# Optimization experiments

Measured on AMD Instinct MI355X. Metric: run time of the kernel, lower is better.

Reference implementation:

```python
import jax, jax.numpy as jnp
import numpy as np

UNITS = 256
IN_DIM = 256
OUT_DIM = 10
TOL = 1e-4
MAX_ITER = 50


def setup_inputs() -> dict:
    key = jax.random.key(0)
    ks = jax.random.split(key, 16)
    B = 65536
    s = 1.0 / np.sqrt(UNITS)
    inp = {
        "x": jax.random.normal(ks[0], (B, IN_DIM), dtype=jnp.float32),
        "w_in": jax.random.normal(ks[1], (IN_DIM, UNITS), dtype=jnp.float32) * s,
        "b_in": jax.random.normal(ks[2], (UNITS,), dtype=jnp.float32) * 0.01,
        "w_out": jax.random.normal(ks[3], (UNITS, OUT_DIM), dtype=jnp.float32) * s,
        "b_out": jax.random.normal(ks[4], (OUT_DIM,), dtype=jnp.float32) * 0.01,
    }
    eye = jnp.eye(UNITS, dtype=jnp.float32)
    for i in range(4):
        # well-conditioned (invertible) implicit-layer weight: I + small perturbation
        inp[f"w{i+1}"] = eye + 0.1 * jax.random.normal(ks[5 + 2 * i], (UNITS, UNITS), dtype=jnp.float32) * s
        inp[f"b{i+1}"] = jax.random.normal(ks[6 + 2 * i], (UNITS,), dtype=jnp.float32) * 0.01
    return inp


def newton_block(x, W, b):
    # Solve z @ W = x + tanh(x) + b by Newton iteration with early exit on ||g||.
    c = x + jnp.tanh(x) + b  # [B, n]
    z0 = x
    g0 = z0 @ W - c

    def cond(state):
        z, g, it = state
        return (it < MAX_ITER) & (jnp.linalg.norm(g) >= TOL)

    def body(state):
        z, g, it = state
        # torch.solve(g[:, :, None], W^T.repeat(B,1,1)): shared matrix -> one solve
        z = z - jnp.linalg.solve(W.T, g.T).T
        g = z @ W - c
        return (z, g, it + 1)

    z, _, _ = jax.lax.while_loop(cond, body, (z0, g0, jnp.asarray(0)))
    z = jax.lax.stop_gradient(z)  # torch loop runs under no_grad
    # final differentiable correction (torch: z = z - (z@W - x - tanh(x) - b))
    return z - (z @ W - c)


def reference(x, w_in, b_in, w1, b1, w2, b2, w3, b3, w4, b4, w_out, b_out):
    z = x @ w_in + b_in
    z = newton_block(z, w1, b1)
    z = newton_block(z, w2, b2)
    z = newton_block(z, w3, b3)
    z = newton_block(z, w4, b4)
    logits = z @ w_out + b_out
    return jax.nn.softmax(logits, axis=1)
```

## Files before the change

kernel.cpp:

```cpp
#include <hip/hip_runtime.h>
#include <hip/hip_fp16.h>
#include <math.h>


typedef __attribute__((ext_vector_type(8))) short short8;
typedef __attribute__((ext_vector_type(4))) float f32x4;

__device__ __forceinline__ float tanh_fast(float x) {
#if __has_builtin(__builtin_amdgcn_exp2f)
  float e = __builtin_amdgcn_exp2f(x * 2.8853900817779268f);
#else
  float e = __expf(2.0f * x);
#endif
  return 1.0f - 2.0f * __builtin_amdgcn_rcpf(e + 1.0f);
}
__device__ __forceinline__ unsigned rn_pair16(float v0, float v1) {
  __half2 h = __floats2half2_rn(v0, v1);
  return *reinterpret_cast<unsigned*>(&h);
}
__device__ __forceinline__ unsigned rtz_pair16(float v0, float v1) {
#if __has_builtin(__builtin_amdgcn_cvt_pkrtz)
  typedef __fp16 h2v __attribute__((ext_vector_type(2)));
  h2v h = __builtin_amdgcn_cvt_pkrtz(v0, v1);
  return *reinterpret_cast<unsigned*>(&h);
#else
  return rn_pair16(v0, v1);
#endif
}

__global__ __launch_bounds__(256) void ns_poly_k(
    const float* __restrict__ w1, const float* __restrict__ w2,
    const float* __restrict__ w3, const float* __restrict__ w4,
    const float* __restrict__ w_in, const float* __restrict__ w_out,
    unsigned* __restrict__ pk) {
  const int bid = blockIdx.x;
  const int t = threadIdx.x;
  if (bid >= 256) {
    int idx = (bid - 256) * 256 + t;
    {
      int kc = idx >> 12;
      int nt = (idx >> 8) & 15;
      int lane = (idx >> 2) & 63;
      int d = idx & 3;
      int n = nt * 16 + (lane & 15);
      int kb = kc * 32 + (lane >> 4) * 8 + d * 2;
      pk[idx] = rn_pair16(w_in[kb * 256 + n], w_in[(kb + 1) * 256 + n]);
    }
    int idx2 = idx + 32768;
    if (idx2 < 34816) {
      int r2 = idx2 - 32768;
      int kc = r2 >> 8;
      int lane = (r2 >> 2) & 63;
      int d = r2 & 3;
      int n = lane & 15;
      int kb = kc * 32 + (lane >> 4) * 8 + d * 2;
      float v0 = (n < 10) ? w_out[kb * 10 + n] : 0.0f;
      float v1 = (n < 10) ? w_out[(kb + 1) * 10 + n] : 0.0f;
      pk[5 * 32768 + r2] = rn_pair16(v0, v1);
    }
    return;
  }
  const int m = bid >> 6;
  const int r0 = (bid & 63) * 4;
  const float* __restrict__ W = (m == 0) ? w1 : (m == 1) ? w2 : (m == 2) ? w3 : w4;
  __shared__ float S[4][256];

#pragma unroll
  for (int i = 0; i < 4; ++i) {
    int e = i * 256 + t;
    int r = e >> 8, c = e & 255;
    S[r][c] = (((r0 + r) == c) ? 6.0f : 0.0f) - W[(r0 + r) * 256 + c];
  }
  __syncthreads();

  const float coef[4] = {-15.0f, 20.0f, -15.0f, 6.0f};
#pragma unroll
  for (int step = 0; step < 4; ++step) {
    float acc[4];
#pragma unroll
    for (int r = 0; r < 4; ++r) acc[r] = 0.0f;
    for (int k = 0; k < 256; k += 4) {
      float4 sv[4];
#pragma unroll
      for (int r = 0; r < 4; ++r) sv[r] = *(const float4*)&S[r][k];
      float wv0 = W[(k + 0) * 256 + t];
      float wv1 = W[(k + 1) * 256 + t];
      float wv2 = W[(k + 2) * 256 + t];
      float wv3 = W[(k + 3) * 256 + t];
#pragma unroll
      for (int r = 0; r < 4; ++r) {
        acc[r] = fmaf(sv[r].x, wv0, acc[r]);
        acc[r] = fmaf(sv[r].y, wv1, acc[r]);
        acc[r] = fmaf(sv[r].z, wv2, acc[r]);
        acc[r] = fmaf(sv[r].w, wv3, acc[r]);
      }
    }
    __syncthreads();
    float cdiag = coef[step];
#pragma unroll
    for (int r = 0; r < 4; ++r)
      S[r][t] = acc[r] + (((r0 + r) == t) ? cdiag : 0.0f);
    __syncthreads();
  }

  const int kc = r0 >> 5;
  const int quad = (r0 >> 3) & 3;
  const int d0 = (r0 & 7) >> 1;
#pragma unroll
  for (int i = 0; i < 2; ++i) {
    int q = i * 256 + t;
    int nt = q >> 5;
    int n16 = (q >> 1) & 15;
    int dd = q & 1;
    int n = nt * 16 + n16;
    int lane = quad * 16 + n16;
    unsigned word = rn_pair16(S[2 * dd][n], S[2 * dd + 1][n]);
    pk[(m + 1) * 32768 + kc * 4096 + nt * 256 + lane * 4 + (d0 + dd)] = word;
  }
}

#define MFMA_PHASE(ACC, S)                                                     \
  {                                                                            \
    const unsigned short* pl = zpl + (S) * 16384;                              \
    _Pragma("unroll") for (int mt = 0; mt < 4; ++mt)                           \
        ACC[mt] = (f32x4){0.f, 0.f, 0.f, 0.f};                                 \
    _Pragma("unroll") for (int kc = 0; kc < 8; ++kc) {                         \
      short8 zf[4];                                                            \
      _Pragma("unroll") for (int mt = 0; mt < 4; ++mt)                         \
          zf[mt] = *(const short8*)&pl[rd_base[mt] + ((rd_pm[mt] ^ (kc * 4)) * 8)]; \
      _Pragma("unroll") for (int mt = 0; mt < 4; ++mt)                         \
          ACC[mt] = __builtin_amdgcn_mfma_f32_16x16x32_f16(wreg[kc], zf[mt],   \
                                                           ACC[mt], 0, 0, 0); \
    }                                                                          \
  }

#define EPI_PHASE(ACC, S, BN, BI, DOTANH)                                      \
  {                                                                            \
    unsigned short* pl = zpl + (S) * 16384;                                    \
    float4 bn4 = make_float4(0.f, 0.f, 0.f, 0.f);                              \
    float4 bi4 = make_float4(0.f, 0.f, 0.f, 0.f);                              \
    if (DOTANH) bn4 = *(const float4*)((BN) + colb);                           \
    if ((BI) != nullptr) bi4 = *(const float4*)((BI) + colb);                  \
    _Pragma("unroll") for (int mt = 0; mt < 4; ++mt) {                         \
      float v0 = ACC[mt][0] + bi4.x;                                           \
      float v1 = ACC[mt][1] + bi4.y;                                           \
      float v2 = ACC[mt][2] + bi4.z;                                           \
      float v3 = ACC[mt][3] + bi4.w;                                           \
      if (DOTANH) {                                                            \
        v0 = v0 + tanh_fast(v0) + bn4.x;                                       \
        v1 = v1 + tanh_fast(v1) + bn4.y;                                       \
        v2 = v2 + tanh_fast(v2) + bn4.z;                                       \
        v3 = v3 + tanh_fast(v3) + bn4.w;                                       \
      }                                                                        \
      uint2 zp;                                                                \
      zp.x = rtz_pair16(v0, v1);                                               \
      zp.y = rtz_pair16(v2, v3);                                               \
      *(uint2*)&pl[wr_off[mt]] = zp;                                           \
    }                                                                          \
  }

__global__ __launch_bounds__(1024, 4) void fused2_k(
    const float* __restrict__ x, const unsigned* __restrict__ pk,
    const float* __restrict__ b_in,
    const float* __restrict__ b1, const float* __restrict__ b2,
    const float* __restrict__ b3, const float* __restrict__ b4,
    const float* __restrict__ b_out, float* __restrict__ out) {
  __shared__ unsigned short zpl[4 * 64 * 256];
  const int t = threadIdx.x;
  const int ln = t & 63;
  const int wv = t >> 6;
  const int quad = ln >> 4;
  const int n16 = ln & 15;
  const int grow0 = blockIdx.x * 256;

#pragma unroll
  for (int i = 0; i < 16; ++i) {
    int e = i * 4096 + t * 4;
    int r = e >> 8, c = e & 255;
    float4 v = *(const float4*)(x + (grow0 + r) * 256 + c);
    int g = r >> 6, rl = r & 63;
    int idx = g * 16384 + rl * 256 + (((c >> 3) ^ (rl & 31)) * 8) + (c & 7);
    uint2 zp;
    zp.x = rtz_pair16(v.x, v.y);
    zp.y = rtz_pair16(v.z, v.w);
    *(uint2*)&zpl[idx] = zp;
  }

  const int colb = wv * 16 + quad * 4;
  int rd_base[4], rd_pm[4], wr_off[4];
#pragma unroll
  for (int mt = 0; mt < 4; ++mt) {
    int mm = mt * 16 + n16;
    rd_base[mt] = mm * 256;
    rd_pm[mt] = quad ^ (mm & 31);
    wr_off[mt] = mm * 256 + (((colb >> 3) ^ (mm & 31)) * 8) + (colb & 7);
  }

  __syncthreads();

  f32x4 accA[4], accB[4];

  for (int layer = 0; layer < 5; ++layer) {
    const unsigned* pkl = pk + layer * 32768 + wv * 256 + ln * 4;
    short8 wreg[8];
#pragma unroll
    for (int kc = 0; kc < 8; ++kc) wreg[kc] = *(const short8*)(pkl + kc * 4096);

    if (layer > 0) {
      const float* bnp = (layer == 1) ? b1 : (layer == 2) ? b2 : (layer == 3) ? b3 : b4;
      const float* bip = (layer == 1) ? b_in : nullptr;
      EPI_PHASE(accB, 3, bnp, bip, true);
    }
    MFMA_PHASE(accA, 0);
    __syncthreads();

    const float* bn = (layer == 0) ? b1 : (layer == 1) ? b2 : (layer == 2) ? b3 : b4;
    const float* bi0 = (layer == 0) ? b_in : nullptr;
    const bool dt = (layer < 4);

    EPI_PHASE(accA, 0, bn, bi0, dt);
    MFMA_PHASE(accB, 1);
    __syncthreads();
    EPI_PHASE(accB, 1, bn, bi0, dt);
    MFMA_PHASE(accA, 2);
    __syncthreads();
    EPI_PHASE(accA, 2, bn, bi0, dt);
    MFMA_PHASE(accB, 3);
    __syncthreads();
  }
  EPI_PHASE(accB, 3, (const float*)nullptr, (const float*)nullptr, false);
  __syncthreads();

  {
    const int g = wv >> 2;
    const int kw = wv & 3;
    f32x4 lacc[4];
#pragma unroll
    for (int mt = 0; mt < 4; ++mt) lacc[mt] = (f32x4){0.f, 0.f, 0.f, 0.f};
    const unsigned* pw = pk + 5 * 32768 + ln * 4;
    const unsigned short* pl = zpl + g * 16384;
#pragma unroll
    for (int kk = 0; kk < 2; ++kk) {
      int kc = kw * 2 + kk;
      short8 wh = *(const short8*)(pw + kc * 256);
#pragma unroll
      for (int mt = 0; mt < 4; ++mt) {
        short8 zf = *(const short8*)&pl[rd_base[mt] + ((rd_pm[mt] ^ (kc * 4)) * 8)];
        lacc[mt] = __builtin_amdgcn_mfma_f32_16x16x32_f16(wh, zf, lacc[mt], 0, 0, 0);
      }
    }
    __syncthreads();
    float* pbuf = (float*)zpl;
#pragma unroll
    for (int mt = 0; mt < 4; ++mt) {
      int addr = g * 4096 + kw * 1024 + (mt * 16 + n16) * 16 + quad * 4;
      *(f32x4*)&pbuf[addr] = lacc[mt];
    }
    __syncthreads();
    if (t < 256) {
      int g2 = t >> 6;
      int rl = t & 63;
      float lg[10];
      float mx = -1e30f;
#pragma unroll
      for (int j = 0; j < 10; ++j) {
        float s = b_out[j];
#pragma unroll
        for (int k2 = 0; k2 < 4; ++k2) s += pbuf[g2 * 4096 + k2 * 1024 + rl * 16 + j];
        lg[j] = s;
        mx = fmaxf(mx, s);
      }
      float sum = 0.f;
#pragma unroll
      for (int j = 0; j < 10; ++j) {
        lg[j] = __expf(lg[j] - mx);
        sum += lg[j];
      }
      float inv = 1.0f / sum;
      float* op = out + (grow0 + t) * 10;
#pragma unroll
      for (int j = 0; j < 10; ++j) op[j] = lg[j] * inv;
    }
  }
}

extern "C" void kernel_launch(void* const* d_in, const int* in_sizes, int n_in,
                              void* d_out, int out_size, void* d_ws, size_t ws_size,
                              hipStream_t stream) {
  const float* x     = (const float*)d_in[0];
  const float* w_in  = (const float*)d_in[1];
  const float* b_in  = (const float*)d_in[2];
  const float* w_out = (const float*)d_in[3];
  const float* b_out = (const float*)d_in[4];
  const float* w1 = (const float*)d_in[5];
  const float* b1 = (const float*)d_in[6];
  const float* w2 = (const float*)d_in[7];
  const float* b2 = (const float*)d_in[8];
  const float* w3 = (const float*)d_in[9];
  const float* b3 = (const float*)d_in[10];
  const float* w4 = (const float*)d_in[11];
  const float* b4 = (const float*)d_in[12];
  float* out = (float*)d_out;

  unsigned* pk = (unsigned*)d_ws;

  ns_poly_k<<<384, 256, 0, stream>>>(w1, w2, w3, w4, w_in, w_out, pk);
  fused2_k<<<256, 1024, 0, stream>>>(x, pk, b_in, b1, b2, b3, b4, b_out, out);
}
```

Before: 212.9 us.

## Restructure fused kernel to 4-wave blocks with 64-column per-wave weight tiles

```diff
diff --git a/kernel.cpp b/kernel.cpp
--- a/kernel.cpp
+++ b/kernel.cpp
@@ -119,154 +119,160 @@
   }
 }
 
-#define MFMA_PHASE(ACC, S)                                                     \
+#define M_PHASE(PL)                                                            \
   {                                                                            \
-    const unsigned short* pl = zpl + (S) * 16384;                              \
     _Pragma("unroll") for (int mt = 0; mt < 4; ++mt)                           \
-        ACC[mt] = (f32x4){0.f, 0.f, 0.f, 0.f};                                 \
+      _Pragma("unroll") for (int nt = 0; nt < 4; ++nt)                         \
+        acc[mt][nt] = (f32x4){0.f, 0.f, 0.f, 0.f};                             \
     _Pragma("unroll") for (int kc = 0; kc < 8; ++kc) {                         \
       short8 zf[4];                                                            \
+      _Pragma("unroll") for (int mt = 0; mt < 4; ++mt) {                       \
+        int mm = mt * 16 + n16;                                                \
+        zf[mt] = *(const short8*)&(PL)[mm * 256 + (((kc * 4 + quad) ^ (mm & 31)) * 8)]; \
+      }                                                                        \
       _Pragma("unroll") for (int mt = 0; mt < 4; ++mt)                         \
-          zf[mt] = *(const short8*)&pl[rd_base[mt] + ((rd_pm[mt] ^ (kc * 4)) * 8)]; \
-      _Pragma("unroll") for (int mt = 0; mt < 4; ++mt)                         \
-          ACC[mt] = __builtin_amdgcn_mfma_f32_16x16x32_f16(wreg[kc], zf[mt],   \
-                                                           ACC[mt], 0, 0, 0); \
+        _Pragma("unroll") for (int nt = 0; nt < 4; ++nt)                       \
+          acc[mt][nt] = __builtin_amdgcn_mfma_f32_16x16x32_f16(                \
+              wreg[nt][kc], zf[mt], acc[mt][nt], 0, 0, 0);                     \
+      __builtin_amdgcn_sched_barrier(0);                                       \
     }                                                                          \
   }
 
-#define EPI_PHASE(ACC, S, BN, BI, DOTANH)                                      \
+#define E_PHASE(PL, BN, BI, DOTANH)                                            \
   {                                                                            \
-    unsigned short* pl = zpl + (S) * 16384;                                    \
-    float4 bn4 = make_float4(0.f, 0.f, 0.f, 0.f);                              \
-    float4 bi4 = make_float4(0.f, 0.f, 0.f, 0.f);                              \
-    if (DOTANH) bn4 = *(const float4*)((BN) + colb);                           \
-    if ((BI) != nullptr) bi4 = *(const float4*)((BI) + colb);                  \
-    _Pragma("unroll") for (int mt = 0; mt < 4; ++mt) {                         \
-      float v0 = ACC[mt][0] + bi4.x;                                           \
-      float v1 = ACC[mt][1] + bi4.y;                                           \
-      float v2 = ACC[mt][2] + bi4.z;                                           \
-      float v3 = ACC[mt][3] + bi4.w;                                           \
-      if (DOTANH) {                                                            \
-        v0 = v0 + tanh_fast(v0) + bn4.x;                                       \
-        v1 = v1 + tanh_fast(v1) + bn4.y;                                       \
-        v2 = v2 + tanh_fast(v2) + bn4.z;                                       \
-        v3 = v3 + tanh_fast(v3) + bn4.w;                                       \
+    _Pragma("unroll") for (int nt = 0; nt < 4; ++nt) {                         \
+      int colb = wv * 64 + nt * 16 + quad * 4;                                 \
+      float4 bi4 = make_float4(0.f, 0.f, 0.f, 0.f);                            \
+      float4 bn4 = make_float4(0.f, 0.f, 0.f, 0.f);                            \
+      if ((BI) != nullptr) bi4 = *(const float4*)((BI) + colb);                \
+      if (DOTANH) bn4 = *(const float4*)((BN) + colb);                         \
+      _Pragma("unroll") for (int mt = 0; mt < 4; ++mt) {                       \
+        int row = mt * 16 + n16;                                               \
+        float v0 = acc[mt][nt][0] + bi4.x;                                     \
+        float v1 = acc[mt][nt][1] + bi4.y;                                     \
+        float v2 = acc[mt][nt][2] + bi4.z;                                     \
+        float v3 = acc[mt][nt][3] + bi4.w;                                     \
+        if (DOTANH) {                                                          \
+          v0 = v0 + tanh_fast(v0) + bn4.x;                                     \
+          v1 = v1 + tanh_fast(v1) + bn4.y;                                     \
+          v2 = v2 + tanh_fast(v2) + bn4.z;                                     \
+          v3 = v3 + tanh_fast(v3) + bn4.w;                                     \
+        }                                                                      \
+        int idx = row * 256 + (((colb >> 3) ^ (row & 31)) * 8) + (colb & 7);   \
+        uint2 zp;                                                              \
+        zp.x = rtz_pair16(v0, v1);                                             \
+        zp.y = rtz_pair16(v2, v3);                                             \
+        *(uint2*)&(PL)[idx] = zp;                                              \
       }                                                                        \
-      uint2 zp;                                                                \
-      zp.x = rtz_pair16(v0, v1);                                               \
-      zp.y = rtz_pair16(v2, v3);                                               \
-      *(uint2*)&pl[wr_off[mt]] = zp;                                           \
     }                                                                          \
   }
 
-__global__ __launch_bounds__(1024, 4) void fused2_k(
+#define LOAD_WREG(LAYER)                                                       \
+  {                                                                            \
+    const unsigned* pkl = pk + (LAYER) * 32768 + wv * 1024 + ln * 4;           \
+    _Pragma("unroll") for (int nt = 0; nt < 4; ++nt)                           \
+      _Pragma("unroll") for (int kc = 0; kc < 8; ++kc)                         \
+        wreg[nt][kc] = *(const short8*)(pkl + kc * 4096 + nt * 256);           \
+  }
+
+__global__ __launch_bounds__(256)
+__attribute__((amdgpu_waves_per_eu(2, 2)))
+void fused3_k(
     const float* __restrict__ x, const unsigned* __restrict__ pk,
     const float* __restrict__ b_in,
     const float* __restrict__ b1, const float* __restrict__ b2,
     const float* __restrict__ b3, const float* __restrict__ b4,
     const float* __restrict__ b_out, float* __restrict__ out) {
-  __shared__ unsigned short zpl[4 * 64 * 256];
+  __shared__ unsigned short zpl[2 * 64 * 256];
   const int t = threadIdx.x;
   const int ln = t & 63;
   const int wv = t >> 6;
   const int quad = ln >> 4;
   const int n16 = ln & 15;
-  const int grow0 = blockIdx.x * 256;
-
-#pragma unroll
-  for (int i = 0; i < 16; ++i) {
-    int e = i * 4096 + t * 4;
+  const int grow0 = blockIdx.x * 128;
+
+  short8 wreg[4][8];
+  f32x4 acc[4][4];
+
+  LOAD_WREG(0);
+
+#pragma unroll
+  for (int i = 0; i < 32; ++i) {
+    int e = i * 1024 + t * 4;
     int r = e >> 8, c = e & 255;
     float4 v = *(const float4*)(x + (grow0 + r) * 256 + c);
-    int g = r >> 6, rl = r & 63;
-    int idx = g * 16384 + rl * 256 + (((c >> 3) ^ (rl & 31)) * 8) + (c & 7);
+    int u = r >> 6, rl = r & 63;
+    int idx = u * 16384 + rl * 256 + (((c >> 3) ^ (rl & 31)) * 8) + (c & 7);
     uint2 zp;
     zp.x = rtz_pair16(v.x, v.y);
     zp.y = rtz_pair16(v.z, v.w);
     *(uint2*)&zpl[idx] = zp;
   }
-
-  const int colb = wv * 16 + quad * 4;
-  int rd_base[4], rd_pm[4], wr_off[4];
-#pragma unroll
-  for (int mt = 0; mt < 4; ++mt) {
-    int mm = mt * 16 + n16;
-    rd_base[mt] = mm * 256;
-    rd_pm[mt] = quad ^ (mm & 31);
-    wr_off[mt] = mm * 256 + (((colb >> 3) ^ (mm & 31)) * 8) + (colb & 7);
-  }
-
   __syncthreads();
 
-  f32x4 accA[4], accB[4];
+  unsigned short* pl0 = zpl;
+  unsigned short* pl1 = zpl + 16384;
+  const float* bnv[4] = {b1, b2, b3, b4};
 
   for (int layer = 0; layer < 5; ++layer) {
-    const unsigned* pkl = pk + layer * 32768 + wv * 256 + ln * 4;
-    short8 wreg[8];
-#pragma unroll
-    for (int kc = 0; kc < 8; ++kc) wreg[kc] = *(const short8*)(pkl + kc * 4096);
-
-    if (layer > 0) {
-      const float* bnp = (layer == 1) ? b1 : (layer == 2) ? b2 : (layer == 3) ? b3 : b4;
-      const float* bip = (layer == 1) ? b_in : nullptr;
-      EPI_PHASE(accB, 3, bnp, bip, true);
-    }
-    MFMA_PHASE(accA, 0);
-    __syncthreads();
-
-    const float* bn = (layer == 0) ? b1 : (layer == 1) ? b2 : (layer == 2) ? b3 : b4;
+    const float* bn = (layer < 4) ? bnv[layer] : nullptr;
     const float* bi0 = (layer == 0) ? b_in : nullptr;
     const bool dt = (layer < 4);
 
-    EPI_PHASE(accA, 0, bn, bi0, dt);
-    MFMA_PHASE(accB, 1);
-    __syncthreads();
-    EPI_PHASE(accB, 1, bn, bi0, dt);
-    MFMA_PHASE(accA, 2);
-    __syncthreads();
-    EPI_PHASE(accA, 2, bn, bi0, dt);
-    MFMA_PHASE(accB, 3);
-    __syncthreads();
-  }
-  EPI_PHASE(accB, 3, (const float*)nullptr, (const float*)nullptr, false);
+    M_PHASE(pl0);
+    __syncthreads();
+    E_PHASE(pl0, bn, bi0, dt);
+    M_PHASE(pl1);
+    __syncthreads();
+    if (layer < 4) LOAD_WREG(layer + 1);
+    E_PHASE(pl1, bn, bi0, dt);
+  }
   __syncthreads();
 
   {
-    const int g = wv >> 2;
-    const int kw = wv & 3;
-    f32x4 lacc[4];
-#pragma unroll
-    for (int mt = 0; mt < 4; ++mt) lacc[mt] = (f32x4){0.f, 0.f, 0.f, 0.f};
+    f32x4 lacc[2][4];
+#pragma unroll
+    for (int u = 0; u < 2; ++u)
+#pragma unroll
+      for (int mt = 0; mt < 4; ++mt) lacc[u][mt] = (f32x4){0.f, 0.f, 0.f, 0.f};
     const unsigned* pw = pk + 5 * 32768 + ln * 4;
-    const unsigned short* pl = zpl + g * 16384;
 #pragma unroll
     for (int kk = 0; kk < 2; ++kk) {
-      int kc = kw * 2 + kk;
+      int kc = wv * 2 + kk;
       short8 wh = *(const short8*)(pw + kc * 256);
 #pragma unroll
+      for (int u = 0; u < 2; ++u) {
+        const unsigned short* pl = zpl + u * 16384;
+#pragma unroll
+        for (int mt = 0; mt < 4; ++mt) {
+          int mm = mt * 16 + n16;
+          short8 zf = *(const short8*)&pl[mm * 256 + (((kc * 4 + quad) ^ (mm & 31)) * 8)];
+          lacc[u][mt] = __builtin_amdgcn_mfma_f32_16x16x32_f16(wh, zf, lacc[u][mt], 0, 0, 0);
+        }
+      }
+    }
+    __syncthreads();
+#pragma unroll
+    for (int u = 0; u < 2; ++u) {
+      float* pbuf = (float*)(zpl + u * 16384);
+#pragma unroll
       for (int mt = 0; mt < 4; ++mt) {
-        short8 zf = *(const short8*)&pl[rd_base[mt] + ((rd_pm[mt] ^ (kc * 4)) * 8)];
-        lacc[mt] = __builtin_amdgcn_mfma_f32_16x16x32_f16(wh, zf, lacc[mt], 0, 0, 0);
-      }
-    }
-    __syncthreads();
-    float* pbuf = (float*)zpl;
-#pragma unroll
-    for (int mt = 0; mt < 4; ++mt) {
-      int addr = g * 4096 + kw * 1024 + (mt * 16 + n16) * 16 + quad * 4;
-      *(f32x4*)&pbuf[addr] = lacc[mt];
-    }
-    __syncthreads();
-    if (t < 256) {
-      int g2 = t >> 6;
+        int addr = wv * 1024 + (mt * 16 + n16) * 16 + quad * 4;
+        *(f32x4*)&pbuf[addr] = lacc[u][mt];
+      }
+    }
+    __syncthreads();
+    if (t < 128) {
+      int u = t >> 6;
       int rl = t & 63;
+      const float* pbuf = (const float*)(zpl + u * 16384);
       float lg[10];
       float mx = -1e30f;
 #pragma unroll
       for (int j = 0; j < 10; ++j) {
         float s = b_out[j];
 #pragma unroll
-        for (int k2 = 0; k2 < 4; ++k2) s += pbuf[g2 * 4096 + k2 * 1024 + rl * 16 + j];
+        for (int w2 = 0; w2 < 4; ++w2) s += pbuf[w2 * 1024 + rl * 16 + j];
         lg[j] = s;
         mx = fmaxf(mx, s);
       }
@@ -305,5 +311,5 @@
   unsigned* pk = (unsigned*)d_ws;
 
   ns_poly_k<<<384, 256, 0, stream>>>(w1, w2, w3, w4, w_in, w_out, pk);
-  fused2_k<<<256, 1024, 0, stream>>>(x, pk, b_in, b1, b2, b3, b4, b_out, out);
-}
+  fused3_k<<<512, 256, 0, stream>>>(x, pk, b_in, b1, b2, b3, b4, b_out, out);
+}
```

New measurement: 205.6 us. 3.4% less time.
